# Optimization experiments

Measured on AMD Instinct MI355X. Metric: run time of the kernel, lower is better.

Reference implementation:

```python
import jax, jax.numpy as jnp
import numpy as np

B, S, D = 64, 2048, 512


def setup_inputs() -> dict:
    key = jax.random.key(0)
    k1, k2, k3, k4 = jax.random.split(key, 4)
    decoder_output = jax.random.normal(k1, (B, 1, D), dtype=jnp.float32)
    encoder_output = jax.random.normal(k2, (B, S, D), dtype=jnp.float32)
    # W_a_tanh: Dense(D) applied to concat([dec, enc]) of width 2D
    scale_w = 1.0 / np.sqrt(2 * D)
    W_t = jax.random.normal(k3, (2 * D, D), dtype=jnp.float32) * scale_w
    b_t = jnp.zeros((D,), dtype=jnp.float32)
    # v_a: Dense(1)
    v_a = jax.random.normal(k4, (D, 1), dtype=jnp.float32) * (1.0 / np.sqrt(D))
    b_v = jnp.zeros((1,), dtype=jnp.float32)
    return {
        "decoder_output": decoder_output,
        "encoder_output": encoder_output,
        "W_t": W_t,
        "b_t": b_t,
        "v_a": v_a,
        "b_v": b_v,
    }


def reference(decoder_output, encoder_output, W_t, b_t, v_a, b_v):
    # concat-variant Luong attention
    dec = jnp.broadcast_to(decoder_output, encoder_output.shape)       # [B,S,D]
    concated = jnp.concatenate((dec, encoder_output), axis=-1)          # [B,S,2D]
    hidden = jnp.tanh(jnp.einsum('bse,ed->bsd', concated, W_t) + b_t)   # [B,S,D]
    score = (jnp.einsum('bsd,do->bso', hidden, v_a) + b_v)              # [B,S,1]
    score = jnp.transpose(score, (0, 2, 1))                             # [B,1,S]
    alignment_vector = jax.nn.softmax(score, axis=2)                    # [B,1,S]
    context_vector = jnp.matmul(alignment_vector, encoder_output)       # [B,1,D]
    return (context_vector, alignment_vector)
```

## Files before the change

kernel.cpp:

```cpp
#include <hip/hip_runtime.h>

#define BB 64
#define SS 2048
#define DD 512

typedef __attribute__((ext_vector_type(8))) short bf16x8;
typedef __attribute__((ext_vector_type(4))) float f32x4;

__device__ __forceinline__ unsigned f2bf(float f) {
    unsigned u = __float_as_uint(f);
    u += 0x7FFFu + ((u >> 16) & 1u);
    return u >> 16;
}

__device__ __forceinline__ float fast_tanh(float x) {
    float ax = fabsf(x);
    float e = __expf(-2.0f * ax);
    float t = (1.0f - e) * __builtin_amdgcn_rcpf(1.0f + e);
    return x < 0.0f ? -t : t;
}

__global__ void prep_w(const float* __restrict__ W, short* __restrict__ Bt) {
    __shared__ float tile[64][65];
    int kt = blockIdx.x >> 3;
    int nt = blockIdx.x & 7;
    int t = threadIdx.x;
    int c = t & 63;
    int rbase = (t >> 6) * 16;
    #pragma unroll
    for (int i = 0; i < 16; ++i) {
        int r = rbase + i;
        tile[r][c] = W[(size_t)(512 + kt * 64 + r) * DD + nt * 64 + c];
    }
    __syncthreads();
    #pragma unroll
    for (int i = 0; i < 16; ++i) {
        int r = rbase + i;
        Bt[(size_t)(nt * 64 + r) * DD + kt * 64 + c] = (short)f2bf(tile[c][r]);
    }
}

__global__ void prep_p(const float* __restrict__ dec, const float* __restrict__ W,
                       const float* __restrict__ bt, float* __restrict__ p) {
    int b = blockIdx.x;
    int d = blockIdx.y * 256 + threadIdx.x;
    float acc = bt[d];
    const float* dv = dec + (size_t)b * DD;
    #pragma unroll 8
    for (int e = 0; e < DD; ++e)
        acc += dv[e] * W[(size_t)e * DD + d];
    p[(size_t)b * DD + d] = acc;
}

__global__ __launch_bounds__(1024, 4)
void fused_k(const float* __restrict__ enc, const short* __restrict__ Bt,
             const float* __restrict__ p, const float* __restrict__ va,
             float* __restrict__ score, float* __restrict__ ml,
             float* __restrict__ pctx) {
    __shared__ char smem[65536 + 2048 + 256];
    char* AhiB = smem;
    float (*red)[512] = (float (*)[512])smem;
    float (*sp)[32]   = (float (*)[32])(smem + 65536);
    float* elds       = (float*)(smem + 67584);

    const int tid  = threadIdx.x;
    const int wave = tid >> 6;
    const int lane = tid & 63;
    const int lm   = lane & 15;
    const int lq   = lane >> 4;
    const int wm   = wave >> 3;
    const int wn   = wave & 7;
    const int blk  = blockIdx.x;
    const int b    = blk >> 5;
    const size_t m0 = (size_t)blk * 64;

    const int srow = tid >> 4;
    const int sc   = tid & 15;
    const unsigned srowB = (unsigned)srow * 1024u;
    const unsigned swsr  = (unsigned)(srow & 7) << 4;
    const float* aptr = enc + (m0 + (size_t)srow) * DD + sc * 4;

    const unsigned swlm = (unsigned)(lm & 7) << 4;
    const unsigned arow0 = (unsigned)(wm * 32 + lm) * 1024u;
    const unsigned arow1 = arow0 + 16u * 1024u;
    const short* Bw = Bt + (size_t)(wn * 64 + lm) * DD + lq * 8;

    f32x4 acc[2][4];
    #pragma unroll
    for (int i = 0; i < 2; ++i)
        #pragma unroll
        for (int j = 0; j < 4; ++j)
            acc[i][j] = (f32x4){0.f, 0.f, 0.f, 0.f};

    f32x4 stg[8];
    #pragma unroll
    for (int s = 0; s < 4; ++s)
        stg[s] = *(const f32x4*)(aptr + s * 64);
    {
        uint2 hv;
        hv.x = f2bf(stg[0].x) | (f2bf(stg[0].y) << 16);
        hv.y = f2bf(stg[0].z) | (f2bf(stg[0].w) << 16);
        *(uint2*)(AhiB + (srowB + ((sc * 8u) ^ swsr))) = hv;
    }
    __syncthreads();

    #pragma unroll
    for (int kt = 0; kt < 8; ++kt) {
        if (kt < 4)
            stg[kt + 4] = *(const f32x4*)(aptr + (kt + 4) * 64);

        const unsigned kb = (unsigned)kt * 128u;
        bf16x8 af[2][2];
        af[0][0] = *(const bf16x8*)(AhiB + arow0 + ((kb + 0u  + lq * 16u) ^ swlm));
        af[0][1] = *(const bf16x8*)(AhiB + arow0 + ((kb + 64u + lq * 16u) ^ swlm));
        af[1][0] = *(const bf16x8*)(AhiB + arow1 + ((kb + 0u  + lq * 16u) ^ swlm));
        af[1][1] = *(const bf16x8*)(AhiB + arow1 + ((kb + 64u + lq * 16u) ^ swlm));

        #pragma unroll
        for (int nf = 0; nf < 4; ++nf) {
            const short* bp = Bw + nf * 16 * DD + kt * 64;
            bf16x8 b0 = *(const bf16x8*)(bp);
            bf16x8 b1 = *(const bf16x8*)(bp + 32);
            acc[0][nf] = __builtin_amdgcn_mfma_f32_16x16x32_bf16(af[0][0], b0, acc[0][nf], 0, 0, 0);
            acc[1][nf] = __builtin_amdgcn_mfma_f32_16x16x32_bf16(af[1][0], b0, acc[1][nf], 0, 0, 0);
            acc[0][nf] = __builtin_amdgcn_mfma_f32_16x16x32_bf16(af[0][1], b1, acc[0][nf], 0, 0, 0);
            acc[1][nf] = __builtin_amdgcn_mfma_f32_16x16x32_bf16(af[1][1], b1, acc[1][nf], 0, 0, 0);
        }

        if (kt < 7) {
            f32x4 x = stg[kt + 1];
            uint2 hv;
            hv.x = f2bf(x.x) | (f2bf(x.y) << 16);
            hv.y = f2bf(x.z) | (f2bf(x.w) << 16);
            *(uint2*)(AhiB + (srowB + (((unsigned)((kt + 1) * 128) + sc * 8u) ^ swsr))) = hv;
        }
        __syncthreads();
    }

    const float* pb = p + (size_t)b * DD;
    float rowsum[2][4];
    #pragma unroll
    for (int mf = 0; mf < 2; ++mf)
        #pragma unroll
        for (int r = 0; r < 4; ++r) rowsum[mf][r] = 0.f;

    #pragma unroll
    for (int nf = 0; nf < 4; ++nf) {
        int n = wn * 64 + nf * 16 + lm;
        float pv = pb[n];
        float vv = va[n];
        #pragma unroll
        for (int mf = 0; mf < 2; ++mf)
            #pragma unroll
            for (int r = 0; r < 4; ++r)
                rowsum[mf][r] += fast_tanh(pv + acc[mf][nf][r]) * vv;
    }
    #pragma unroll
    for (int mf = 0; mf < 2; ++mf)
        #pragma unroll
        for (int r = 0; r < 4; ++r) {
            float s = rowsum[mf][r];
            s += __shfl_xor(s, 1);
            s += __shfl_xor(s, 2);
            s += __shfl_xor(s, 4);
            s += __shfl_xor(s, 8);
            rowsum[mf][r] = s;
        }
    if (lm == 0) {
        #pragma unroll
        for (int mf = 0; mf < 2; ++mf)
            #pragma unroll
            for (int r = 0; r < 4; ++r)
                sp[wave][mf * 16 + lq * 4 + r] = rowsum[mf][r];
    }
    __syncthreads();

    if (tid < 64) {
        const int base = (tid >> 5) * 8;
        const int rl = tid & 31;
        float s = 0.f;
        #pragma unroll
        for (int w = 0; w < 8; ++w) s += sp[base + w][rl];
        score[m0 + tid] = s;
        float mx = s;
        #pragma unroll
        for (int off = 32; off > 0; off >>= 1) mx = fmaxf(mx, __shfl_xor(mx, off));
        float e = __expf(s - mx);
        float l = e;
        #pragma unroll
        for (int off = 32; off > 0; off >>= 1) l += __shfl_xor(l, off);
        elds[tid] = e;
        if (tid == 0) {
            ml[(size_t)blk * 2]     = mx;
            ml[(size_t)blk * 2 + 1] = l;
        }
    }
    __syncthreads();

    {
        float ev = elds[srow];
        #pragma unroll
        for (int s = 0; s < 8; ++s) {
            float v0 = ev * stg[s].x;
            float v1 = ev * stg[s].y;
            float v2 = ev * stg[s].z;
            float v3 = ev * stg[s].w;
            v0 += __shfl_xor(v0, 16); v0 += __shfl_xor(v0, 32);
            v1 += __shfl_xor(v1, 16); v1 += __shfl_xor(v1, 32);
            v2 += __shfl_xor(v2, 16); v2 += __shfl_xor(v2, 32);
            v3 += __shfl_xor(v3, 16); v3 += __shfl_xor(v3, 32);
            if (lane < 16)
                *(f32x4*)(&red[wave][s * 64 + sc * 4]) = (f32x4){v0, v1, v2, v3};
        }
    }
    __syncthreads();
    if (tid < 512) {
        float v = 0.f;
        #pragma unroll
        for (int w = 0; w < 16; ++w) v += red[w][tid];
        pctx[(size_t)blk * 512 + tid] = v;
    }
}

__global__ void combine_k(const float* __restrict__ score, const float* __restrict__ ml,
                          const float* __restrict__ pctx, float* __restrict__ ctx,
                          float* __restrict__ align) {
    __shared__ float sc[32];
    __shared__ float MB, LB;
    const int b = blockIdx.x, tid = threadIdx.x;
    if (tid < 32) sc[tid] = ml[(size_t)(b * 32 + tid) * 2];
    __syncthreads();
    if (tid == 0) {
        float M = sc[0];
        #pragma unroll
        for (int i = 1; i < 32; ++i) M = fmaxf(M, sc[i]);
        float L = 0.f;
        for (int i = 0; i < 32; ++i) {
            float w = __expf(sc[i] - M);
            L += w * ml[(size_t)(b * 32 + i) * 2 + 1];
            sc[i] = w;
        }
        MB = M;
        LB = L;
    }
    __syncthreads();
    const float M = MB, Linv = 1.0f / LB;
    float a0 = 0.f, a1 = 0.f;
    for (int i = 0; i < 32; ++i) {
        float w = sc[i];
        const float* pc = pctx + (size_t)(b * 32 + i) * 512;
        a0 += w * pc[tid];
        a1 += w * pc[tid + 256];
    }
    ctx[(size_t)b * DD + tid]       = a0 * Linv;
    ctx[(size_t)b * DD + tid + 256] = a1 * Linv;
    const float* sr = score + (size_t)b * SS;
    float* al = align + (size_t)b * SS;
    #pragma unroll
    for (int i = 0; i < 8; ++i) {
        int s = i * 256 + tid;
        al[s] = __expf(sr[s] - M) * Linv;
    }
}

extern "C" void kernel_launch(void* const* d_in, const int* in_sizes, int n_in,
                              void* d_out, int out_size, void* d_ws, size_t ws_size,
                              hipStream_t stream) {
    const float* dec = (const float*)d_in[0];
    const float* enc = (const float*)d_in[1];
    const float* W   = (const float*)d_in[2];
    const float* bt  = (const float*)d_in[3];
    const float* va  = (const float*)d_in[4];

    float* out   = (float*)d_out;
    float* ctx   = out;
    float* align = out + BB * DD;

    char*  ws    = (char*)d_ws;
    short* Bt    = (short*)ws;
    float* p     = (float*)(ws + 524288);
    float* score = (float*)(ws + 655360);
    float* ml    = (float*)(ws + 1179648);
    float* pctx  = (float*)(ws + 1196032);

    prep_w<<<64, 256, 0, stream>>>(W, Bt);
    prep_p<<<dim3(BB, 2), 256, 0, stream>>>(dec, W, bt, p);
    fused_k<<<BB * 32, 1024, 0, stream>>>(enc, Bt, p, va, score, ml, pctx);
    combine_k<<<BB, 256, 0, stream>>>(score, ml, pctx, ctx, align);
}
```

Baseline: 656.2 us.

## Halve A-tile k-step and re-read encoder rows for the context sum

The main GEMM loop now runs 16 k-steps of 32 instead of 8 of 64. Each thread stages float2 values in a 4-deep ring rather than holding all eight f32x4 encoder chunks in registers. The context partial sum no longer reuses those register-held values. It re-reads encoder rows from global memory (likely L2-resident) with a column-parallel loop and a two-way LDS reduction. The goal is to cut register pressure and shuffle-based reductions, at the cost of twice as many barriers, smaller per-step loads, and a second global read of the encoder tile.

```diff
diff --git a/kernel.cpp b/kernel.cpp
--- a/kernel.cpp
+++ b/kernel.cpp
@@ -78,7 +78,7 @@
     const int sc   = tid & 15;
     const unsigned srowB = (unsigned)srow * 1024u;
     const unsigned swsr  = (unsigned)(srow & 7) << 4;
-    const float* aptr = enc + (m0 + (size_t)srow) * DD + sc * 4;
+    const float* aptr = enc + (m0 + (size_t)srow) * DD + sc * 2;
 
     const unsigned swlm = (unsigned)(lm & 7) << 4;
     const unsigned arow0 = (unsigned)(wm * 32 + lm) * 1024u;
@@ -92,47 +92,36 @@
         for (int j = 0; j < 4; ++j)
             acc[i][j] = (f32x4){0.f, 0.f, 0.f, 0.f};
 
-    f32x4 stg[8];
-    #pragma unroll
-    for (int s = 0; s < 4; ++s)
-        stg[s] = *(const f32x4*)(aptr + s * 64);
+    float2 stg[4];
+    stg[0] = *(const float2*)(aptr);
+    stg[1] = *(const float2*)(aptr + 32);
+    stg[2] = *(const float2*)(aptr + 64);
     {
-        uint2 hv;
-        hv.x = f2bf(stg[0].x) | (f2bf(stg[0].y) << 16);
-        hv.y = f2bf(stg[0].z) | (f2bf(stg[0].w) << 16);
-        *(uint2*)(AhiB + (srowB + ((sc * 8u) ^ swsr))) = hv;
-    }
-    __syncthreads();
-
-    #pragma unroll
-    for (int kt = 0; kt < 8; ++kt) {
-        if (kt < 4)
-            stg[kt + 4] = *(const f32x4*)(aptr + (kt + 4) * 64);
-
-        const unsigned kb = (unsigned)kt * 128u;
-        bf16x8 af[2][2];
-        af[0][0] = *(const bf16x8*)(AhiB + arow0 + ((kb + 0u  + lq * 16u) ^ swlm));
-        af[0][1] = *(const bf16x8*)(AhiB + arow0 + ((kb + 64u + lq * 16u) ^ swlm));
-        af[1][0] = *(const bf16x8*)(AhiB + arow1 + ((kb + 0u  + lq * 16u) ^ swlm));
-        af[1][1] = *(const bf16x8*)(AhiB + arow1 + ((kb + 64u + lq * 16u) ^ swlm));
+        unsigned hv = f2bf(stg[0].x) | (f2bf(stg[0].y) << 16);
+        *(unsigned*)(AhiB + (srowB + (((unsigned)sc * 4u) ^ swsr))) = hv;
+    }
+    __syncthreads();
+
+    #pragma unroll
+    for (int kt = 0; kt < 16; ++kt) {
+        if (kt < 13)
+            stg[(kt + 3) & 3] = *(const float2*)(aptr + (kt + 3) * 32);
+
+        const unsigned kb = (unsigned)kt * 64u;
+        bf16x8 af0 = *(const bf16x8*)(AhiB + arow0 + ((kb + lq * 16u) ^ swlm));
+        bf16x8 af1 = *(const bf16x8*)(AhiB + arow1 + ((kb + lq * 16u) ^ swlm));
 
         #pragma unroll
         for (int nf = 0; nf < 4; ++nf) {
-            const short* bp = Bw + nf * 16 * DD + kt * 64;
-            bf16x8 b0 = *(const bf16x8*)(bp);
-            bf16x8 b1 = *(const bf16x8*)(bp + 32);
-            acc[0][nf] = __builtin_amdgcn_mfma_f32_16x16x32_bf16(af[0][0], b0, acc[0][nf], 0, 0, 0);
-            acc[1][nf] = __builtin_amdgcn_mfma_f32_16x16x32_bf16(af[1][0], b0, acc[1][nf], 0, 0, 0);
-            acc[0][nf] = __builtin_amdgcn_mfma_f32_16x16x32_bf16(af[0][1], b1, acc[0][nf], 0, 0, 0);
-            acc[1][nf] = __builtin_amdgcn_mfma_f32_16x16x32_bf16(af[1][1], b1, acc[1][nf], 0, 0, 0);
-        }
-
-        if (kt < 7) {
-            f32x4 x = stg[kt + 1];
-            uint2 hv;
-            hv.x = f2bf(x.x) | (f2bf(x.y) << 16);
-            hv.y = f2bf(x.z) | (f2bf(x.w) << 16);
-            *(uint2*)(AhiB + (srowB + (((unsigned)((kt + 1) * 128) + sc * 8u) ^ swsr))) = hv;
+            bf16x8 bfr = *(const bf16x8*)(Bw + nf * 16 * DD + kt * 32);
+            acc[0][nf] = __builtin_amdgcn_mfma_f32_16x16x32_bf16(af0, bfr, acc[0][nf], 0, 0, 0);
+            acc[1][nf] = __builtin_amdgcn_mfma_f32_16x16x32_bf16(af1, bfr, acc[1][nf], 0, 0, 0);
+        }
+
+        if (kt < 15) {
+            float2 x = stg[(kt + 1) & 3];
+            unsigned hv = f2bf(x.x) | (f2bf(x.y) << 16);
+            *(unsigned*)(AhiB + (srowB + (((unsigned)((kt + 1) * 64) + sc * 4u) ^ swsr))) = hv;
         }
         __syncthreads();
     }
@@ -198,28 +187,18 @@
     __syncthreads();
 
     {
-        float ev = elds[srow];
-        #pragma unroll
-        for (int s = 0; s < 8; ++s) {
-            float v0 = ev * stg[s].x;
-            float v1 = ev * stg[s].y;
-            float v2 = ev * stg[s].z;
-            float v3 = ev * stg[s].w;
-            v0 += __shfl_xor(v0, 16); v0 += __shfl_xor(v0, 32);
-            v1 += __shfl_xor(v1, 16); v1 += __shfl_xor(v1, 32);
-            v2 += __shfl_xor(v2, 16); v2 += __shfl_xor(v2, 32);
-            v3 += __shfl_xor(v3, 16); v3 += __shfl_xor(v3, 32);
-            if (lane < 16)
-                *(f32x4*)(&red[wave][s * 64 + sc * 4]) = (f32x4){v0, v1, v2, v3};
-        }
-    }
-    __syncthreads();
-    if (tid < 512) {
+        const int d = tid & 511;
+        const int g = tid >> 9;
+        const float* erow = enc + (m0 + (size_t)g * 32) * DD + d;
         float v = 0.f;
         #pragma unroll
-        for (int w = 0; w < 16; ++w) v += red[w][tid];
-        pctx[(size_t)blk * 512 + tid] = v;
-    }
+        for (int s = 0; s < 32; ++s)
+            v += elds[g * 32 + s] * erow[(size_t)s * DD];
+        red[g][d] = v;
+    }
+    __syncthreads();
+    if (tid < 512)
+        pctx[(size_t)blk * 512 + tid] = red[0][tid] + red[1][tid];
 }
 
 __global__ void combine_k(const float* __restrict__ score, const float* __restrict__ ml,
```

Result: no change. 654.8 us (-0.2%).
